# Kernel tuning notes

Measured on AMD Instinct MI355X. Metric: run time of the kernel, lower is better.

## Reference

```python
import jax, jax.numpy as jnp
import numpy as np

B, N, I, H, NT = 512, 21, 256, 1024, 5  # batch, nodes, input, hidden, node types
EPS = 1e-12


def setup_inputs() -> dict:
    key = jax.random.key(0)
    ks = jax.random.split(key, 8)
    stdv = 1.0 / np.sqrt(H)
    return {
        "input": jax.random.normal(ks[0], (B, N, I), jnp.float32),
        "hx": 0.1 * jax.random.normal(ks[1], (B, N, H), jnp.float32),
        "cx": 0.1 * jax.random.normal(ks[2], (B, N, H), jnp.float32),
        "G": jnp.eye(N, dtype=jnp.float32) + 0.01 * jax.random.normal(ks[3], (N, N), jnp.float32),
        "weight_ih": jax.random.uniform(ks[4], (NT, 4 * H, I), jnp.float32, -stdv, stdv),
        "weight_hh": jax.random.uniform(ks[5], (NT, 4 * H, H), jnp.float32, -stdv, stdv),
        "bias_hh": jax.random.uniform(ks[6], (NT, 4 * H), jnp.float32, -stdv, stdv),
        "node_types": jax.random.randint(ks[7], (N,), 0, NT),
        "t": 3,
    }


def _l1_normalize_rows(g):
    # torch.nn.functional.normalize(g, p=1, dim=1)
    return g / jnp.maximum(jnp.sum(jnp.abs(g), axis=1, keepdims=True), EPS)


def _clockwork_phase(hidden_size, dtype):
    p = jnp.arange(hidden_size, dtype=dtype)
    p = p / p[-1] * 8.0 + 1.0
    return jnp.floor(p)  # values in {1..9}


def reference(input, hx, cx, G, weight_ih, weight_hh, bias_hh, node_types, t):
    # learn_influence=True -> gx = L1-row-normalized G
    gx = _l1_normalize_rows(G)

    # per-node-type weight gather: [N, 4H, I], [N, 4H, H], [N, 4H]
    w_ih = weight_ih[node_types]
    w_hh = weight_hh[node_types]
    b_hh = bias_hh[node_types]

    # gmm: einsum('ndo,bnd->bno', w.transpose(-2,-1), x) == einsum('noi,bni->bno', w, x)
    gates = (jnp.einsum('noi,bni->bno', w_ih, input)
             + jnp.einsum('noh,bnh->bno', w_hh, hx)
             + b_hh)
    # graph influence: matmul(gx, gates) over node dim -> [B, N, 4H]
    gates = jnp.einsum('mn,bno->bmo', gx, gates)

    ingate, forgetgate, cellgate, outgate = jnp.split(gates, 4, axis=2)
    ingate = jax.nn.sigmoid(ingate)
    forgetgate = jax.nn.sigmoid(forgetgate)
    cellgate = jnp.tanh(cellgate)
    outgate = jax.nn.sigmoid(outgate)

    phase = _clockwork_phase(hx.shape[-1], cx.dtype)
    c_mask = (jnp.remainder(jnp.float32(t) + 1.0, phase) < 0.01).astype(cx.dtype)

    cy = c_mask * (forgetgate * cx + ingate * cellgate) + (1.0 - c_mask) * cx
    hy = outgate * jnp.tanh(cy)

    # gx = gx + G_add (=0), then re-normalized because learn_influence=True
    gx_out = _l1_normalize_rows(gx)
    return hy, cy, gx_out
```

## Files before the change

kernel.cpp:

```cpp
#include <hip/hip_runtime.h>
#include <hip/hip_bf16.h>
#include <stdint.h>


typedef __bf16 bf16_t;
typedef __bf16 bf16x8 __attribute__((ext_vector_type(8)));
typedef float f32x4 __attribute__((ext_vector_type(4)));

#define NB 512
#define NN 21
#define NI 256
#define NH 1024
#define KDIM 1280
#define ODIM 4096
#define BNH (512ull * 21 * 1024)

__device__ inline void gld16(const void* g, const void* l) {
  __builtin_amdgcn_global_load_lds(
      (const __attribute__((address_space(1))) unsigned int*)g,
      (__attribute__((address_space(3))) unsigned int*)l, 16, 0, 0);
}

__device__ inline float sigmoid_fast(float x) {
  return 1.0f / (1.0f + __expf(-x));
}
__device__ inline float tanh_fast(float x) {
  float ax = fabsf(x);
  float e = __expf(2.0f * ax);
  float t = 1.0f - 2.0f / (e + 1.0f);
  return copysignf(t, x);
}

__device__ inline void wg_barrier() {
  asm volatile("" ::: "memory");
  __builtin_amdgcn_s_barrier();
  asm volatile("" ::: "memory");
}

__global__ __launch_bounds__(256) void pack_all(
    const float* __restrict__ wih, const float* __restrict__ whh,
    const float* __restrict__ input, const float* __restrict__ hx,
    const float* __restrict__ G, bf16_t* __restrict__ Wc,
    bf16_t* __restrict__ Xc, float* __restrict__ gxw,
    float* __restrict__ gxout) {
  const int bx = blockIdx.x;
  const int tid = threadIdx.x;
  if (bx < 12800) {
    int c = bx * 256 + tid;
    int k8 = c % (KDIM / 8);
    int row = c / (KDIM / 8);
    int k = k8 * 8;
    const float* src = (k < NI) ? (wih + (size_t)row * NI + k)
                                : (whh + (size_t)row * NH + (k - NI));
    float4 a = *(const float4*)src;
    float4 b = *(const float4*)(src + 4);
    bf16x8 o;
    o[0] = (bf16_t)a.x; o[1] = (bf16_t)a.y; o[2] = (bf16_t)a.z; o[3] = (bf16_t)a.w;
    o[4] = (bf16_t)b.x; o[5] = (bf16_t)b.y; o[6] = (bf16_t)b.z; o[7] = (bf16_t)b.w;
    *(bf16x8*)&Wc[(size_t)c * 8] = o;
  } else if (bx < 19520) {
    int c = (bx - 12800) * 256 + tid;
    int k8 = c % (KDIM / 8);
    int rest = c / (KDIM / 8);
    int n = rest / NB;
    int b = rest % NB;
    int k = k8 * 8;
    const float* src = (k < NI) ? (input + ((size_t)b * NN + n) * NI + k)
                                : (hx + ((size_t)b * NN + n) * NH + (k - NI));
    float4 a = *(const float4*)src;
    float4 d = *(const float4*)(src + 4);
    bf16x8 o;
    o[0] = (bf16_t)a.x; o[1] = (bf16_t)a.y; o[2] = (bf16_t)a.z; o[3] = (bf16_t)a.w;
    o[4] = (bf16_t)d.x; o[5] = (bf16_t)d.y; o[6] = (bf16_t)d.z; o[7] = (bf16_t)d.w;
    *(bf16x8*)&Xc[(size_t)c * 8] = o;
  } else {
    int m = tid;
    if (m < NN) {
      float s = 0.f;
      for (int j = 0; j < NN; j++) s += fabsf(G[m * NN + j]);
      s = fmaxf(s, 1e-12f);
      float row[NN];
      float s2 = 0.f;
      for (int j = 0; j < NN; j++) {
        row[j] = G[m * NN + j] / s;
        s2 += fabsf(row[j]);
      }
      s2 = fmaxf(s2, 1e-12f);
      for (int j = 0; j < NN; j++) {
        gxw[m * NN + j] = row[j];
        gxout[m * NN + j] = row[j] / s2;
      }
    }
  }
}

__global__ __launch_bounds__(512, 2) void gemm_bt(
    const bf16_t* __restrict__ Xc, const bf16_t* __restrict__ Wc,
    const float* __restrict__ bhh, const int* __restrict__ node_types,
    bf16_t* __restrict__ gates) {
  __shared__ char lds[4 * 32768];

  const int n = blockIdx.z;
  const int tau = node_types[n];
  const bf16_t* A = Xc + (size_t)n * NB * KDIM;
  const bf16_t* Bw = Wc + (size_t)tau * ODIM * KDIM;

  const int tid = threadIdx.x;
  const int lane = tid & 63;
  const int w = tid >> 6;
  const int wm = (w & 1) * 128;
  const int wn = (w >> 1) * 64;
  const int r = lane & 15;
  const int quad = lane >> 4;

  const int m0 = blockIdx.y * 256;
  const int n0 = blockIdx.x * 256;

  const int ga = ((wm + r) >> 1) & 3;
  const int gb = ((wn + r) >> 1) & 3;
  const int aoff = (wm + r) * 64 + ((quad ^ ga) * 16);
  const int boff = 16384 + (wn + r) * 64 + ((quad ^ gb) * 16);

  const int ca = w * 128 + lane;
  const int cb = ca + 64;
  const int rA0 = ca >> 2, cA0 = (ca & 3) ^ ((rA0 >> 1) & 3);
  const int rA1 = cb >> 2, cA1 = (cb & 3) ^ ((rA1 >> 1) & 3);
  const bf16_t* gA0 = A + (size_t)(m0 + rA0) * KDIM + cA0 * 8;
  const bf16_t* gA1 = A + (size_t)(m0 + rA1) * KDIM + cA1 * 8;
  const bf16_t* gB0 = Bw + (size_t)(n0 + rA0) * KDIM + cA0 * 8;
  const bf16_t* gB1 = Bw + (size_t)(n0 + rA1) * KDIM + cA1 * 8;
  const int dA0 = ca * 16, dA1 = cb * 16;

  f32x4 acc[8][4];
#pragma unroll
  for (int i = 0; i < 8; i++)
#pragma unroll
    for (int j = 0; j < 4; j++) acc[i][j] = {0.f, 0.f, 0.f, 0.f};

  {
    char* L0 = lds;
    char* L1 = lds + 32768;
    gld16(gA0, L0 + dA0);          gld16(gA1, L0 + dA1);
    gld16(gB0, L0 + 16384 + dA0);  gld16(gB1, L0 + 16384 + dA1);
    gld16(gA0 + 32, L1 + dA0);         gld16(gA1 + 32, L1 + dA1);
    gld16(gB0 + 32, L1 + 16384 + dA0); gld16(gB1 + 32, L1 + 16384 + dA1);
    asm volatile("s_waitcnt vmcnt(4)" ::: "memory");
    wg_barrier();
  }

  for (int t = 0; t < 40; ++t) {
    const char* P = lds + (t & 3) * 32768;
    char* Wd = lds + ((t + 2) & 3) * 32768;
    const bool st = (t < 38);
    const int kk = (t + 2) * 32;
    bf16x8 a0[4], a1[4], b0[4];

#pragma unroll
    for (int i = 0; i < 4; i++) a0[i] = *(const bf16x8*)(P + aoff + i * 1024);
#pragma unroll
    for (int j = 0; j < 4; j++) b0[j] = *(const bf16x8*)(P + boff + j * 1024);
    if (st) { gld16(gA0 + kk, Wd + dA0); gld16(gA1 + kk, Wd + dA1); }
    wg_barrier();
    asm volatile("s_waitcnt lgkmcnt(0)" ::: "memory");
    __builtin_amdgcn_sched_barrier(0);
    __builtin_amdgcn_s_setprio(1);
#pragma unroll
    for (int i = 0; i < 4; i++)
#pragma unroll
      for (int j = 0; j < 4; j++)
        acc[i][j] = __builtin_amdgcn_mfma_f32_16x16x32_bf16(a0[i], b0[j], acc[i][j], 0, 0, 0);
    __builtin_amdgcn_s_setprio(0);
    wg_barrier();

#pragma unroll
    for (int i = 0; i < 4; i++) a1[i] = *(const bf16x8*)(P + aoff + 4096 + i * 1024);
    if (st) { gld16(gB0 + kk, Wd + 16384 + dA0); gld16(gB1 + kk, Wd + 16384 + dA1); }
    wg_barrier();
    asm volatile("s_waitcnt lgkmcnt(0)" ::: "memory");
    __builtin_amdgcn_sched_barrier(0);
    __builtin_amdgcn_s_setprio(1);
#pragma unroll
    for (int i = 0; i < 4; i++)
#pragma unroll
      for (int j = 0; j < 4; j++)
        acc[4 + i][j] = __builtin_amdgcn_mfma_f32_16x16x32_bf16(a1[i], b0[j], acc[4 + i][j], 0, 0, 0);
    __builtin_amdgcn_s_setprio(0);
    if (t < 38)       asm volatile("s_waitcnt vmcnt(4)" ::: "memory");
    else if (t == 38) asm volatile("s_waitcnt vmcnt(0)" ::: "memory");
    wg_barrier();
  }

  float bv[4];
#pragma unroll
  for (int j = 0; j < 4; j++) bv[j] = bhh[tau * ODIM + n0 + wn + j * 16 + r];
#pragma unroll
  for (int i = 0; i < 8; i++) {
    int brow = m0 + wm + i * 16 + quad * 4;
#pragma unroll
    for (int j = 0; j < 4; j++) {
      int o = n0 + wn + j * 16 + r;
#pragma unroll
      for (int reg = 0; reg < 4; reg++) {
        int b = brow + reg;
        gates[((size_t)b * NN + n) * ODIM + o] = (bf16_t)(acc[i][j][reg] + bv[j]);
      }
    }
  }
}

template <int M0C, int CH>
__device__ inline void mix_chunk(const bf16_t (*gs)[4][256],
                                 const float* __restrict__ gx,
                                 const float* __restrict__ cx,
                                 float* __restrict__ out, int b, int h, int tid,
                                 bool cmask) {
  float a[CH][4];
#pragma unroll
  for (int mm = 0; mm < CH; mm++) {
    a[mm][0] = 0.f; a[mm][1] = 0.f; a[mm][2] = 0.f; a[mm][3] = 0.f;
  }
  for (int nn = 0; nn < NN; nn++) {
    float v0 = (float)gs[nn][0][tid];
    float v1 = (float)gs[nn][1][tid];
    float v2 = (float)gs[nn][2][tid];
    float v3 = (float)gs[nn][3][tid];
#pragma unroll
    for (int mm = 0; mm < CH; mm++) {
      float wgt = gx[(M0C + mm) * NN + nn];
      a[mm][0] = fmaf(wgt, v0, a[mm][0]);
      a[mm][1] = fmaf(wgt, v1, a[mm][1]);
      a[mm][2] = fmaf(wgt, v2, a[mm][2]);
      a[mm][3] = fmaf(wgt, v3, a[mm][3]);
    }
  }
#pragma unroll
  for (int mm = 0; mm < CH; mm++) {
    int m = M0C + mm;
    size_t off = ((size_t)b * NN + m) * NH + h;
    float c0 = cx[off];
    float ig = sigmoid_fast(a[mm][0]);
    float fg = sigmoid_fast(a[mm][1]);
    float cg = tanh_fast(a[mm][2]);
    float og = sigmoid_fast(a[mm][3]);
    float c = cmask ? fmaf(fg, c0, ig * cg) : c0;
    out[off] = og * tanh_fast(c);
    out[BNH + off] = c;
  }
}

__global__ __launch_bounds__(256) void mix_lstm(const bf16_t* __restrict__ gates,
                                                const float* __restrict__ gx,
                                                const float* __restrict__ cx,
                                                const int* __restrict__ t_ptr,
                                                float* __restrict__ out) {
  __shared__ bf16_t gs[NN][4][256];
  const int tid = threadIdx.x;
  const int b = blockIdx.y;
  const int h0 = blockIdx.x * 256;
  const size_t gb = (size_t)b * NN * ODIM;
  for (int i = tid; i < NN * 4 * 32; i += 256) {
    int nn = i >> 7;
    int rem = i & 127;
    int g = rem >> 5;
    int c = rem & 31;
    *(bf16x8*)&gs[nn][g][c * 8] =
        *(const bf16x8*)&gates[gb + (size_t)nn * ODIM + g * NH + h0 + c * 8];
  }
  __syncthreads();

  const int h = h0 + tid;
  const float tf = (float)(t_ptr[0] + 1);
  float phase = floorf((float)h / 1023.0f * 8.0f + 1.0f);
  bool cmask = fmodf(tf, phase) < 0.01f;

  mix_chunk<0, 11>(gs, gx, cx, out, b, h, tid, cmask);
  mix_chunk<11, 10>(gs, gx, cx, out, b, h, tid, cmask);
}

extern "C" void kernel_launch(void* const* d_in, const int* in_sizes, int n_in,
                              void* d_out, int out_size, void* d_ws, size_t ws_size,
                              hipStream_t stream) {
  const float* input = (const float*)d_in[0];
  const float* hx = (const float*)d_in[1];
  const float* cx = (const float*)d_in[2];
  const float* G = (const float*)d_in[3];
  const float* wih = (const float*)d_in[4];
  const float* whh = (const float*)d_in[5];
  const float* bhh = (const float*)d_in[6];
  const int* node_types = (const int*)d_in[7];
  const int* t = (const int*)d_in[8];
  float* out = (float*)d_out;

  char* ws = (char*)d_ws;
  bf16_t* Wc = (bf16_t*)ws;
  bf16_t* Xc = (bf16_t*)(ws + 52428800);
  bf16_t* gates = (bf16_t*)(ws + 79953920);
  float* gxw = (float*)(ws + 168034304);

  pack_all<<<19521, 256, 0, stream>>>(wih, whh, input, hx, G, Wc, Xc, gxw,
                                      out + 2 * BNH);
  dim3 gg(ODIM / 256, NB / 256, NN);
  gemm_bt<<<gg, 512, 0, stream>>>(Xc, Wc, bhh, node_types, gates);
  dim3 gm(NH / 256, NB);
  mix_lstm<<<gm, 256, 0, stream>>>(gates, gxw, cx, t, out);
}
```

Before: 426.8 us.

## Switch GEMM to 32x32x16 MFMA with new LDS swizzle and one barrier per step

Replaces the 16x16x32 bf16 MFMA tiles with 32x32x16 MFMAs (four by two accumulators of 16 floats per wave) and changes the LDS XOR swizzle to match the new fragment access pattern. The main loop now issues all four global-to-LDS prefetches together and keeps a single workgroup barrier per K step instead of four, removing the split-phase schedule. The aim is fewer LDS reads per MFMA and less synchronisation overhead. The cost is a different scheduling balance and a risk of LDS bank conflicts or reduced overlap.

```diff
diff --git a/kernel.cpp b/kernel.cpp
--- a/kernel.cpp
+++ b/kernel.cpp
@@ -6,6 +6,7 @@
 typedef __bf16 bf16_t;
 typedef __bf16 bf16x8 __attribute__((ext_vector_type(8)));
 typedef float f32x4 __attribute__((ext_vector_type(4)));
+typedef float f32x16 __attribute__((ext_vector_type(16)));
 
 #define NB 512
 #define NN 21
@@ -110,32 +111,43 @@
   const int w = tid >> 6;
   const int wm = (w & 1) * 128;
   const int wn = (w >> 1) * 64;
-  const int r = lane & 15;
-  const int quad = lane >> 4;
+  const int lr = lane & 31;
+  const int hi = lane >> 5;
 
   const int m0 = blockIdx.y * 256;
   const int n0 = blockIdx.x * 256;
 
-  const int ga = ((wm + r) >> 1) & 3;
-  const int gb = ((wn + r) >> 1) & 3;
-  const int aoff = (wm + r) * 64 + ((quad ^ ga) * 16);
-  const int boff = 16384 + (wn + r) * 64 + ((quad ^ gb) * 16);
+  int aoffs[4], boffs[2];
+#pragma unroll
+  for (int i = 0; i < 4; i++) {
+    int R = wm + i * 32 + lr;
+    int phys = (hi ^ ((R >> 1) ^ (R >> 3))) & 3;
+    aoffs[i] = R * 64 + phys * 16;
+  }
+#pragma unroll
+  for (int j = 0; j < 2; j++) {
+    int R = wn + j * 32 + lr;
+    int phys = (hi ^ ((R >> 1) ^ (R >> 3))) & 3;
+    boffs[j] = 16384 + R * 64 + phys * 16;
+  }
 
   const int ca = w * 128 + lane;
   const int cb = ca + 64;
-  const int rA0 = ca >> 2, cA0 = (ca & 3) ^ ((rA0 >> 1) & 3);
-  const int rA1 = cb >> 2, cA1 = (cb & 3) ^ ((rA1 >> 1) & 3);
+  const int rA0 = ca >> 2, cA0 = (ca & 3) ^ (((rA0 >> 1) ^ (rA0 >> 3)) & 3);
+  const int rA1 = cb >> 2, cA1 = (cb & 3) ^ (((rA1 >> 1) ^ (rA1 >> 3)) & 3);
   const bf16_t* gA0 = A + (size_t)(m0 + rA0) * KDIM + cA0 * 8;
   const bf16_t* gA1 = A + (size_t)(m0 + rA1) * KDIM + cA1 * 8;
   const bf16_t* gB0 = Bw + (size_t)(n0 + rA0) * KDIM + cA0 * 8;
   const bf16_t* gB1 = Bw + (size_t)(n0 + rA1) * KDIM + cA1 * 8;
   const int dA0 = ca * 16, dA1 = cb * 16;
 
-  f32x4 acc[8][4];
-#pragma unroll
-  for (int i = 0; i < 8; i++)
-#pragma unroll
-    for (int j = 0; j < 4; j++) acc[i][j] = {0.f, 0.f, 0.f, 0.f};
+  f32x16 acc[4][2];
+#pragma unroll
+  for (int i = 0; i < 4; i++)
+#pragma unroll
+    for (int j = 0; j < 2; j++)
+#pragma unroll
+      for (int e = 0; e < 16; e++) acc[i][j][e] = 0.f;
 
   {
     char* L0 = lds;
@@ -150,59 +162,53 @@
 
   for (int t = 0; t < 40; ++t) {
     const char* P = lds + (t & 3) * 32768;
-    char* Wd = lds + ((t + 2) & 3) * 32768;
-    const bool st = (t < 38);
-    const int kk = (t + 2) * 32;
-    bf16x8 a0[4], a1[4], b0[4];
-
-#pragma unroll
-    for (int i = 0; i < 4; i++) a0[i] = *(const bf16x8*)(P + aoff + i * 1024);
-#pragma unroll
-    for (int j = 0; j < 4; j++) b0[j] = *(const bf16x8*)(P + boff + j * 1024);
-    if (st) { gld16(gA0 + kk, Wd + dA0); gld16(gA1 + kk, Wd + dA1); }
-    wg_barrier();
-    asm volatile("s_waitcnt lgkmcnt(0)" ::: "memory");
-    __builtin_amdgcn_sched_barrier(0);
+    bf16x8 af[4][2], bfr[2][2];
+#pragma unroll
+    for (int j = 0; j < 2; j++) {
+      bfr[j][0] = *(const bf16x8*)(P + boffs[j]);
+      bfr[j][1] = *(const bf16x8*)(P + (boffs[j] ^ 32));
+    }
+#pragma unroll
+    for (int i = 0; i < 4; i++) {
+      af[i][0] = *(const bf16x8*)(P + aoffs[i]);
+      af[i][1] = *(const bf16x8*)(P + (aoffs[i] ^ 32));
+    }
+    if (t < 38) {
+      char* Wd = lds + ((t + 2) & 3) * 32768;
+      const int kk = (t + 2) * 32;
+      gld16(gA0 + kk, Wd + dA0);          gld16(gA1 + kk, Wd + dA1);
+      gld16(gB0 + kk, Wd + 16384 + dA0);  gld16(gB1 + kk, Wd + 16384 + dA1);
+    }
     __builtin_amdgcn_s_setprio(1);
 #pragma unroll
     for (int i = 0; i < 4; i++)
 #pragma unroll
-      for (int j = 0; j < 4; j++)
-        acc[i][j] = __builtin_amdgcn_mfma_f32_16x16x32_bf16(a0[i], b0[j], acc[i][j], 0, 0, 0);
-    __builtin_amdgcn_s_setprio(0);
-    wg_barrier();
-
-#pragma unroll
-    for (int i = 0; i < 4; i++) a1[i] = *(const bf16x8*)(P + aoff + 4096 + i * 1024);
-    if (st) { gld16(gB0 + kk, Wd + 16384 + dA0); gld16(gB1 + kk, Wd + 16384 + dA1); }
-    wg_barrier();
-    asm volatile("s_waitcnt lgkmcnt(0)" ::: "memory");
-    __builtin_amdgcn_sched_barrier(0);
-    __builtin_amdgcn_s_setprio(1);
-#pragma unroll
-    for (int i = 0; i < 4; i++)
-#pragma unroll
-      for (int j = 0; j < 4; j++)
-        acc[4 + i][j] = __builtin_amdgcn_mfma_f32_16x16x32_bf16(a1[i], b0[j], acc[4 + i][j], 0, 0, 0);
+      for (int j = 0; j < 2; j++) {
+        acc[i][j] = __builtin_amdgcn_mfma_f32_32x32x16_bf16(af[i][0], bfr[j][0], acc[i][j], 0, 0, 0);
+        acc[i][j] = __builtin_amdgcn_mfma_f32_32x32x16_bf16(af[i][1], bfr[j][1], acc[i][j], 0, 0, 0);
+      }
     __builtin_amdgcn_s_setprio(0);
     if (t < 38)       asm volatile("s_waitcnt vmcnt(4)" ::: "memory");
     else if (t == 38) asm volatile("s_waitcnt vmcnt(0)" ::: "memory");
-    wg_barrier();
-  }
-
-  float bv[4];
-#pragma unroll
-  for (int j = 0; j < 4; j++) bv[j] = bhh[tau * ODIM + n0 + wn + j * 16 + r];
-#pragma unroll
-  for (int i = 0; i < 8; i++) {
-    int brow = m0 + wm + i * 16 + quad * 4;
-#pragma unroll
-    for (int j = 0; j < 4; j++) {
-      int o = n0 + wn + j * 16 + r;
-#pragma unroll
-      for (int reg = 0; reg < 4; reg++) {
-        int b = brow + reg;
-        gates[((size_t)b * NN + n) * ODIM + o] = (bf16_t)(acc[i][j][reg] + bv[j]);
+    if (t < 39) wg_barrier();
+  }
+
+  float bv[2];
+#pragma unroll
+  for (int j = 0; j < 2; j++) bv[j] = bhh[tau * ODIM + n0 + wn + j * 32 + lr];
+#pragma unroll
+  for (int i = 0; i < 4; i++) {
+#pragma unroll
+    for (int j = 0; j < 2; j++) {
+      const int o = n0 + wn + j * 32 + lr;
+#pragma unroll
+      for (int q = 0; q < 4; q++) {
+#pragma unroll
+        for (int rr = 0; rr < 4; rr++) {
+          int b = m0 + wm + i * 32 + rr + 8 * q + 4 * hi;
+          gates[((size_t)b * NN + n) * ODIM + o] =
+              (bf16_t)(acc[i][j][q * 4 + rr] + bv[j]);
+        }
       }
     }
   }
```

Measured after the change: 438.8 us. +2.8%, slower.

## Restructure GEMM to 128x256 tiles with 4 waves and XCD-aware block remap

Applied to the files above, without the earlier changes.

The per-node GEMM moves from 512-thread blocks with 256x256 tiles and a 4-stage 32-wide K ring to 256-thread blocks with 128x256 tiles. Each K step is now 64 wide, split into A and B half-buffers inside a 48KB LDS footprint, and the load and MFMA phases are interleaved across four sub-steps. The launch becomes a flat 1D grid of 1344 blocks, remapped so that blocks dispatched round-robin across the 8 XCDs share node and weight tiles in L2. This is meant to raise occupancy and cache locality, at the cost of more intricate vmcnt bookkeeping and fewer MFMAs per LDS load.

```diff
diff --git a/kernel.cpp b/kernel.cpp
--- a/kernel.cpp
+++ b/kernel.cpp
@@ -94,42 +94,48 @@
   }
 }
 
-__global__ __launch_bounds__(512, 2) void gemm_bt(
+__global__ __launch_bounds__(256, 2) void gemm_bt(
     const bf16_t* __restrict__ Xc, const bf16_t* __restrict__ Wc,
     const float* __restrict__ bhh, const int* __restrict__ node_types,
     bf16_t* __restrict__ gates) {
-  __shared__ char lds[4 * 32768];
-
-  const int n = blockIdx.z;
+  __shared__ char lds[49152];
+
+  const int bid = blockIdx.x;
+  const int l = (bid & 7) * 168 + (bid >> 3);
+  const int n = l / 64;
+  const int rem = l & 63;
+  const int m0 = (rem >> 4) * 128;
+  const int n0 = (rem & 15) * 256;
+
   const int tau = node_types[n];
-  const bf16_t* A = Xc + (size_t)n * NB * KDIM;
-  const bf16_t* Bw = Wc + (size_t)tau * ODIM * KDIM;
+  const bf16_t* An = Xc + (size_t)n * NB * KDIM;
+  const bf16_t* Bt = Wc + (size_t)tau * ODIM * KDIM;
 
   const int tid = threadIdx.x;
   const int lane = tid & 63;
   const int w = tid >> 6;
-  const int wm = (w & 1) * 128;
-  const int wn = (w >> 1) * 64;
   const int r = lane & 15;
   const int quad = lane >> 4;
 
-  const int m0 = blockIdx.y * 256;
-  const int n0 = blockIdx.x * 256;
-
-  const int ga = ((wm + r) >> 1) & 3;
-  const int gb = ((wn + r) >> 1) & 3;
-  const int aoff = (wm + r) * 64 + ((quad ^ ga) * 16);
-  const int boff = 16384 + (wn + r) * 64 + ((quad ^ gb) * 16);
-
-  const int ca = w * 128 + lane;
-  const int cb = ca + 64;
-  const int rA0 = ca >> 2, cA0 = (ca & 3) ^ ((rA0 >> 1) & 3);
-  const int rA1 = cb >> 2, cA1 = (cb & 3) ^ ((rA1 >> 1) & 3);
-  const bf16_t* gA0 = A + (size_t)(m0 + rA0) * KDIM + cA0 * 8;
-  const bf16_t* gA1 = A + (size_t)(m0 + rA1) * KDIM + cA1 * 8;
-  const bf16_t* gB0 = Bw + (size_t)(n0 + rA0) * KDIM + cA0 * 8;
-  const bf16_t* gB1 = Bw + (size_t)(n0 + rA1) * KDIM + cA1 * 8;
-  const int dA0 = ca * 16, dA1 = cb * 16;
+  const int pA = (quad ^ (r & 7)) * 16;
+  const int aoff = r * 128 + pA;
+  const int boff = 16384 + w * 4096 + r * 128 + pA;
+
+  const bf16_t* sAlo[2];
+  const bf16_t* sB0[4];
+#pragma unroll
+  for (int p = 0; p < 2; p++) {
+    int ci = tid + p * 256;
+    int row = ci >> 3, lc = (ci & 7) ^ (row & 7);
+    sAlo[p] = An + (size_t)(m0 + row) * KDIM + lc * 8;
+  }
+#pragma unroll
+  for (int p = 0; p < 4; p++) {
+    int ci = tid + p * 256;
+    int lr = ci >> 3, lc = (ci & 7) ^ (lr & 7);
+    int R0 = (lr >> 5) * 64 + (lr & 31);
+    sB0[p] = Bt + (size_t)(n0 + R0) * KDIM + lc * 8;
+  }
 
   f32x4 acc[8][4];
 #pragma unroll
@@ -138,28 +144,38 @@
     for (int j = 0; j < 4; j++) acc[i][j] = {0.f, 0.f, 0.f, 0.f};
 
   {
-    char* L0 = lds;
-    char* L1 = lds + 32768;
-    gld16(gA0, L0 + dA0);          gld16(gA1, L0 + dA1);
-    gld16(gB0, L0 + 16384 + dA0);  gld16(gB1, L0 + 16384 + dA1);
-    gld16(gA0 + 32, L1 + dA0);         gld16(gA1 + 32, L1 + dA1);
-    gld16(gB0 + 32, L1 + 16384 + dA0); gld16(gB1 + 32, L1 + 16384 + dA1);
-    asm volatile("s_waitcnt vmcnt(4)" ::: "memory");
-    wg_barrier();
-  }
-
-  for (int t = 0; t < 40; ++t) {
-    const char* P = lds + (t & 3) * 32768;
-    char* Wd = lds + ((t + 2) & 3) * 32768;
-    const bool st = (t < 38);
-    const int kk = (t + 2) * 32;
-    bf16x8 a0[4], a1[4], b0[4];
-
-#pragma unroll
-    for (int i = 0; i < 4; i++) a0[i] = *(const bf16x8*)(P + aoff + i * 1024);
-#pragma unroll
-    for (int j = 0; j < 4; j++) b0[j] = *(const bf16x8*)(P + boff + j * 1024);
-    if (st) { gld16(gA0 + kk, Wd + dA0); gld16(gA1 + kk, Wd + dA1); }
+#pragma unroll
+    for (int p = 0; p < 2; p++) gld16(sAlo[p], lds + tid * 16 + p * 4096);
+#pragma unroll
+    for (int p = 0; p < 4; p++) gld16(sB0[p], lds + 16384 + tid * 16 + p * 4096);
+#pragma unroll
+    for (int p = 0; p < 4; p++)
+      gld16(sB0[p] + 32 * KDIM, lds + 32768 + tid * 16 + p * 4096);
+#pragma unroll
+    for (int p = 0; p < 2; p++)
+      gld16(sAlo[p] + 64 * KDIM, lds + 8192 + tid * 16 + p * 4096);
+#pragma unroll
+    for (int p = 0; p < 2; p++) sAlo[p] += 64;
+#pragma unroll
+    for (int p = 0; p < 4; p++) sB0[p] += 64;
+    asm volatile("s_waitcnt vmcnt(6)" ::: "memory");
+    wg_barrier();
+  }
+
+  bf16x8 af[4][2], b0v[2][2], b1v[2][2];
+
+  for (int t = 0; t < 20; ++t) {
+    const bool st = (t < 19);
+#pragma unroll
+    for (int i = 0; i < 4; i++) {
+      af[i][0] = *(const bf16x8*)(lds + (aoff + i * 2048));
+      af[i][1] = *(const bf16x8*)(lds + ((aoff + i * 2048) ^ 64));
+    }
+#pragma unroll
+    for (int j = 0; j < 2; j++) {
+      b0v[j][0] = *(const bf16x8*)(lds + (boff + j * 2048));
+      b0v[j][1] = *(const bf16x8*)(lds + ((boff + j * 2048) ^ 64));
+    }
     wg_barrier();
     asm volatile("s_waitcnt lgkmcnt(0)" ::: "memory");
     __builtin_amdgcn_sched_barrier(0);
@@ -167,14 +183,25 @@
 #pragma unroll
     for (int i = 0; i < 4; i++)
 #pragma unroll
-      for (int j = 0; j < 4; j++)
-        acc[i][j] = __builtin_amdgcn_mfma_f32_16x16x32_bf16(a0[i], b0[j], acc[i][j], 0, 0, 0);
+      for (int j = 0; j < 2; j++) {
+        acc[i][j] = __builtin_amdgcn_mfma_f32_16x16x32_bf16(af[i][0], b0v[j][0], acc[i][j], 0, 0, 0);
+        acc[i][j] = __builtin_amdgcn_mfma_f32_16x16x32_bf16(af[i][1], b0v[j][1], acc[i][j], 0, 0, 0);
+      }
     __builtin_amdgcn_s_setprio(0);
-    wg_barrier();
-
-#pragma unroll
-    for (int i = 0; i < 4; i++) a1[i] = *(const bf16x8*)(P + aoff + 4096 + i * 1024);
-    if (st) { gld16(gB0 + kk, Wd + 16384 + dA0); gld16(gB1 + kk, Wd + 16384 + dA1); }
+    asm volatile("s_waitcnt vmcnt(2)" ::: "memory");
+    wg_barrier();
+
+#pragma unroll
+    for (int j = 0; j < 2; j++) {
+      b1v[j][0] = *(const bf16x8*)(lds + (boff + 16384 + j * 2048));
+      b1v[j][1] = *(const bf16x8*)(lds + ((boff + 16384 + j * 2048) ^ 64));
+    }
+    if (st) {
+#pragma unroll
+      for (int p = 0; p < 2; p++) gld16(sAlo[p], lds + tid * 16 + p * 4096);
+#pragma unroll
+      for (int p = 0; p < 4; p++) gld16(sB0[p], lds + 16384 + tid * 16 + p * 4096);
+    }
     wg_barrier();
     asm volatile("s_waitcnt lgkmcnt(0)" ::: "memory");
     __builtin_amdgcn_sched_barrier(0);
@@ -182,23 +209,72 @@
 #pragma unroll
     for (int i = 0; i < 4; i++)
 #pragma unroll
-      for (int j = 0; j < 4; j++)
-        acc[4 + i][j] = __builtin_amdgcn_mfma_f32_16x16x32_bf16(a1[i], b0[j], acc[4 + i][j], 0, 0, 0);
+      for (int j = 0; j < 2; j++) {
+        acc[i][2 + j] = __builtin_amdgcn_mfma_f32_16x16x32_bf16(af[i][0], b1v[j][0], acc[i][2 + j], 0, 0, 0);
+        acc[i][2 + j] = __builtin_amdgcn_mfma_f32_16x16x32_bf16(af[i][1], b1v[j][1], acc[i][2 + j], 0, 0, 0);
+      }
     __builtin_amdgcn_s_setprio(0);
-    if (t < 38)       asm volatile("s_waitcnt vmcnt(4)" ::: "memory");
-    else if (t == 38) asm volatile("s_waitcnt vmcnt(0)" ::: "memory");
-    wg_barrier();
+    if (st) asm volatile("s_waitcnt vmcnt(6)" ::: "memory");
+    else    asm volatile("s_waitcnt vmcnt(0)" ::: "memory");
+    wg_barrier();
+
+#pragma unroll
+    for (int i = 0; i < 4; i++) {
+      af[i][0] = *(const bf16x8*)(lds + (aoff + 8192 + i * 2048));
+      af[i][1] = *(const bf16x8*)(lds + ((aoff + 8192 + i * 2048) ^ 64));
+    }
+    if (st) {
+#pragma unroll
+      for (int p = 0; p < 4; p++)
+        gld16(sB0[p] + 32 * KDIM, lds + 32768 + tid * 16 + p * 4096);
+    }
+    wg_barrier();
+    asm volatile("s_waitcnt lgkmcnt(0)" ::: "memory");
+    __builtin_amdgcn_sched_barrier(0);
+    __builtin_amdgcn_s_setprio(1);
+#pragma unroll
+    for (int i = 0; i < 4; i++)
+#pragma unroll
+      for (int j = 0; j < 2; j++) {
+        acc[4 + i][2 + j] = __builtin_amdgcn_mfma_f32_16x16x32_bf16(af[i][0], b1v[j][0], acc[4 + i][2 + j], 0, 0, 0);
+        acc[4 + i][2 + j] = __builtin_amdgcn_mfma_f32_16x16x32_bf16(af[i][1], b1v[j][1], acc[4 + i][2 + j], 0, 0, 0);
+      }
+    __builtin_amdgcn_s_setprio(0);
+    wg_barrier();
+
+    if (st) {
+#pragma unroll
+      for (int p = 0; p < 2; p++)
+        gld16(sAlo[p] + 64 * KDIM, lds + 8192 + tid * 16 + p * 4096);
+    }
+    wg_barrier();
+    __builtin_amdgcn_s_setprio(1);
+#pragma unroll
+    for (int i = 0; i < 4; i++)
+#pragma unroll
+      for (int j = 0; j < 2; j++) {
+        acc[4 + i][j] = __builtin_amdgcn_mfma_f32_16x16x32_bf16(af[i][0], b0v[j][0], acc[4 + i][j], 0, 0, 0);
+        acc[4 + i][j] = __builtin_amdgcn_mfma_f32_16x16x32_bf16(af[i][1], b0v[j][1], acc[4 + i][j], 0, 0, 0);
+      }
+    __builtin_amdgcn_s_setprio(0);
+    if (st) asm volatile("s_waitcnt vmcnt(6)" ::: "memory");
+    wg_barrier();
+
+#pragma unroll
+    for (int p = 0; p < 2; p++) sAlo[p] += 64;
+#pragma unroll
+    for (int p = 0; p < 4; p++) sB0[p] += 64;
   }
 
   float bv[4];
 #pragma unroll
-  for (int j = 0; j < 4; j++) bv[j] = bhh[tau * ODIM + n0 + wn + j * 16 + r];
+  for (int j = 0; j < 4; j++) bv[j] = bhh[tau * ODIM + n0 + w * 64 + j * 16 + r];
 #pragma unroll
   for (int i = 0; i < 8; i++) {
-    int brow = m0 + wm + i * 16 + quad * 4;
+    int brow = m0 + i * 16 + quad * 4;
 #pragma unroll
     for (int j = 0; j < 4; j++) {
-      int o = n0 + wn + j * 16 + r;
+      int o = n0 + w * 64 + j * 16 + r;
 #pragma unroll
       for (int reg = 0; reg < 4; reg++) {
         int b = brow + reg;
@@ -299,8 +375,7 @@
 
   pack_all<<<19521, 256, 0, stream>>>(wih, whh, input, hx, G, Wc, Xc, gxw,
                                       out + 2 * BNH);
-  dim3 gg(ODIM / 256, NB / 256, NN);
-  gemm_bt<<<gg, 512, 0, stream>>>(Xc, Wc, bhh, node_types, gates);
+  gemm_bt<<<1344, 256, 0, stream>>>(Xc, Wc, bhh, node_types, gates);
   dim3 gm(NH / 256, NB);
   mix_lstm<<<gm, 256, 0, stream>>>(gates, gxw, cx, t, out);
 }
```

Measured after the change: 417.3 us. -2.2%, faster.
